# Performance work log

Measured on AMD Instinct MI355X. Metric: run time of the kernel, lower is better.

The kernel has to match this reference:

```python
import jax, jax.numpy as jnp
import numpy as np

N_NODES = 100000


def _gcn_conv(x, W, b, src, dst, n_nodes):
    """PyG GCNConv: linear -> symmetric norm (with self-loops) -> scatter-add -> bias."""
    h = x @ W  # [N, out]
    # add self-loops
    loop = jnp.arange(n_nodes, dtype=src.dtype)
    s = jnp.concatenate([src, loop])
    d = jnp.concatenate([dst, loop])
    # degree of target nodes (edge weight = 1)
    deg = jax.ops.segment_sum(jnp.ones_like(d, dtype=h.dtype), d, num_segments=n_nodes)
    dinv = jnp.where(deg > 0, jax.lax.rsqrt(jnp.maximum(deg, 1e-12)), 0.0)
    norm = dinv[s] * dinv[d]  # [E+N]
    msg = h[s] * norm[:, None]  # gather + scale
    out = jax.ops.segment_sum(msg, d, num_segments=n_nodes)
    return out + b


def setup_inputs() -> dict:
    key = jax.random.key(0)
    k1, k2, k3, k4 = jax.random.split(key, 4)
    F_IN, HID, OUT, E = 128, 16, 12, 3200000
    x = jax.random.normal(k1, (N_NODES, F_IN), dtype=jnp.float32)
    edge_index = jax.random.randint(k2, (2, E), 0, N_NODES, dtype=jnp.int64)
    W1 = jax.random.normal(k3, (F_IN, HID), dtype=jnp.float32) / np.sqrt(F_IN)
    b1 = jnp.zeros((HID,), dtype=jnp.float32)
    W2 = jax.random.normal(k4, (HID, OUT), dtype=jnp.float32) / np.sqrt(HID)
    b2 = jnp.zeros((OUT,), dtype=jnp.float32)
    return {"x": x, "edge_index": edge_index, "W1": W1, "b1": b1, "W2": W2, "b2": b2}


def reference(x, edge_index, W1, b1, W2, b2):
    src, dst = edge_index[0], edge_index[1]
    h = _gcn_conv(x, W1, b1, src, dst, N_NODES)
    h = jax.nn.relu(h)
    # dropout is identity at inference
    h = _gcn_conv(h, W2, b2, src, dst, N_NODES)
    return jax.nn.log_softmax(h, axis=1)
```

## Files before the change

### kernel.cpp

```cpp
#include <hip/hip_runtime.h>
#include <hip/hip_fp16.h>

#define N_FIN 128
#define N_HID 16
#define N_OUT 12
#define NBLK  1024
#define BN    512
#define STCAP 3200
#define SCAP  17152

__global__ __launch_bounds__(256) void k_binsort(const int* __restrict__ src,
                                                 const int* __restrict__ dst,
                                                 unsigned* __restrict__ hist,
                                                 unsigned* __restrict__ lstart,
                                                 unsigned* __restrict__ entries,
                                                 int E, int chunk, int NB) {
  __shared__ unsigned lh[256];
  __shared__ unsigned cur[256];
  __shared__ unsigned stage[STCAP];
  int t = threadIdx.x, blk = blockIdx.x;
  for (int b = t; b < NB; b += 256) lh[b] = 0u;
  __syncthreads();
  int clo = blk * chunk, chi = min(E, clo + chunk);
  for (int j = clo + t; j < chi; j += 256) atomicAdd(&lh[dst[j] >> 9], 1u);
  __syncthreads();
  unsigned v = (t < NB) ? lh[t] : 0u;
  cur[t] = v;
  __syncthreads();
#pragma unroll
  for (int off = 1; off < 256; off <<= 1) {
    unsigned y = (t >= off) ? cur[t - off] : 0u;
    __syncthreads();
    cur[t] += y;
    __syncthreads();
  }
  unsigned excl = cur[t] - v;
  if (t < NB) {
    hist[(size_t)t * NBLK + blk]   = v;
    lstart[(size_t)t * NBLK + blk] = excl;
  }
  cur[t] = excl;
  __syncthreads();
  for (int j = clo + t; j < chi; j += 256) {
    int d = dst[j];
    int b = d >> 9;
    unsigned p = atomicAdd(&cur[b], 1u);
    stage[p] = ((unsigned)src[j] << 9) | (unsigned)(d & (BN - 1));
  }
  __syncthreads();
  int n = chi - clo;
  for (int i = t; i < n; i += 256) entries[clo + i] = stage[i];
}

__global__ __launch_bounds__(256) void k_scan1(const unsigned* __restrict__ in,
                                               unsigned* __restrict__ out,
                                               unsigned* __restrict__ bsum, int M) {
  __shared__ unsigned s[256];
  int t = threadIdx.x, i = blockIdx.x * 256 + t;
  unsigned v = (i < M) ? in[i] : 0u;
  s[t] = v;
  __syncthreads();
#pragma unroll
  for (int off = 1; off < 256; off <<= 1) {
    unsigned y = (t >= off) ? s[t - off] : 0u;
    __syncthreads();
    s[t] += y;
    __syncthreads();
  }
  if (i < M) out[i] = s[t] - v;
  if (t == 255) bsum[blockIdx.x] = s[255];
}

__global__ __launch_bounds__(1024) void k_scan2(unsigned* __restrict__ bsum, int nb) {
  __shared__ unsigned s[1024];
  int t = threadIdx.x;
  unsigned v = (t < nb) ? bsum[t] : 0u;
  s[t] = v;
  __syncthreads();
#pragma unroll
  for (int off = 1; off < 1024; off <<= 1) {
    unsigned y = (t >= off) ? s[t - off] : 0u;
    __syncthreads();
    s[t] += y;
    __syncthreads();
  }
  if (t < nb) bsum[t] = s[t] - v;
}

__global__ __launch_bounds__(256) void k_scan3(unsigned* __restrict__ out,
                                               const unsigned* __restrict__ bsum, int M) {
  int i = blockIdx.x * 256 + threadIdx.x;
  if (i < M) out[i] += bsum[blockIdx.x];
}

__device__ __forceinline__ int frag_search(const unsigned* cum, unsigned i) {
  int lo = 0, hi = 1024;
  while (hi - lo > 1) { int mid = (lo + hi) >> 1; if (cum[mid] <= i) lo = mid; else hi = mid; }
  return lo;
}

__global__ __launch_bounds__(1024) void k_build(const unsigned* __restrict__ entries,
                                                const unsigned* __restrict__ base,
                                                const unsigned* __restrict__ lstart,
                                                unsigned* __restrict__ row_start,
                                                unsigned* __restrict__ deg,
                                                float* __restrict__ dinv,
                                                unsigned* __restrict__ esrc,
                                                int N, int NB, int E, int chunk) {
  __shared__ unsigned cum[1025];
  __shared__ unsigned lst[1024];
  __shared__ unsigned cnt[BN];
  __shared__ unsigned cur[BN];
  __shared__ unsigned raw[SCAP];
  __shared__ unsigned srt[SCAP];
  int t = threadIdx.x, b = blockIdx.x;
  unsigned bstart = base[(size_t)b * NBLK];
  unsigned bend = (b + 1 < NB) ? base[(size_t)(b + 1) * NBLK] : (unsigned)E;
  unsigned tot = bend - bstart;
  cum[t] = base[(size_t)b * NBLK + t] - bstart;
  lst[t] = lstart[(size_t)b * NBLK + t];
  if (t == 0) cum[1024] = tot;
  if (t < BN) cnt[t] = 0u;
  __syncthreads();
  bool fits = (tot <= SCAP);
  for (unsigned i = t; i < tot; i += 1024) {
    int f = frag_search(cum, i);
    unsigned en = entries[(size_t)f * chunk + lst[f] + (i - cum[f])];
    if (fits) raw[i] = en;
    atomicAdd(&cnt[en & (BN - 1)], 1u);
  }
  __syncthreads();
  unsigned v = (t < BN) ? cnt[t] : 0u;
  if (t < BN) cur[t] = v;
  __syncthreads();
#pragma unroll
  for (int off = 1; off < BN; off <<= 1) {
    unsigned y = (t < BN && t >= off) ? cur[t - off] : 0u;
    __syncthreads();
    if (t < BN) cur[t] += y;
    __syncthreads();
  }
  if (t < BN) {
    unsigned excl = cur[t] - v;
    cur[t] = fits ? excl : (bstart + excl);
    int node = b * BN + t;
    if (node < N) {
      row_start[node] = bstart + excl;
      deg[node] = v;
      dinv[node] = rsqrtf((float)(v + 1u));
    }
  }
  __syncthreads();
  if (fits) {
    for (unsigned i = t; i < tot; i += 1024) {
      unsigned en = raw[i];
      unsigned p = atomicAdd(&cur[en & (BN - 1)], 1u);
      srt[p] = en >> 9;
    }
    __syncthreads();
    for (unsigned i = t; i < tot; i += 1024) esrc[bstart + i] = srt[i];
  } else {
    for (unsigned i = t; i < tot; i += 1024) {
      int f = frag_search(cum, i);
      unsigned en = entries[(size_t)f * chunk + lst[f] + (i - cum[f])];
      unsigned p = atomicAdd(&cur[en & (BN - 1)], 1u);
      esrc[p] = en >> 9;
    }
  }
}

__global__ __launch_bounds__(256) void k_gemm1(const float* __restrict__ x,
                                               const float* __restrict__ W1,
                                               const float* __restrict__ dinv,
                                               __half* __restrict__ hs, int N) {
  __shared__ float xs[16][132];
  __shared__ float wT[16][132];
  int t = threadIdx.x;
#pragma unroll
  for (int i = 0; i < 8; ++i) {
    int idx = t + i * 256;
    int k = idx >> 4, c = idx & 15;
    wT[c][k] = W1[idx];
  }
  int row0 = blockIdx.x * 16;
#pragma unroll
  for (int i = 0; i < 2; ++i) {
    int idx = t + i * 256;
    int r = idx >> 5, c4 = idx & 31;
    float4 v = make_float4(0.f, 0.f, 0.f, 0.f);
    if (row0 + r < N) v = *(const float4*)(x + (size_t)(row0 + r) * N_FIN + c4 * 4);
    *(float4*)&xs[r][c4 * 4] = v;
  }
  __syncthreads();
  int col = t & 15, r = t >> 4;
  float acc = 0.f;
#pragma unroll
  for (int kc = 0; kc < 32; ++kc) {
    float4 xv = *(const float4*)&xs[r][kc * 4];
    float4 wv = *(const float4*)&wT[col][kc * 4];
    acc += xv.x * wv.x + xv.y * wv.y + xv.z * wv.z + xv.w * wv.w;
  }
  int row = row0 + r;
  if (row < N) hs[(size_t)row * N_HID + col] = __float2half(dinv[row] * acc);
}

__device__ __forceinline__ float4 h4f(uint2 v) {
  __half2 h0 = *(__half2*)&v.x, h1 = *(__half2*)&v.y;
  float2 f0 = __half22float2(h0), f1 = __half22float2(h1);
  return make_float4(f0.x, f0.y, f1.x, f1.y);
}
#define ACC(a, v) { float4 f = h4f(v); a.x += f.x; a.y += f.y; a.z += f.z; a.w += f.w; }

__global__ __launch_bounds__(256) void k_gagg1(const unsigned* __restrict__ esrc,
                                               const unsigned* __restrict__ row_start,
                                               const unsigned* __restrict__ deg,
                                               const uint2* __restrict__ hs,
                                               const float* __restrict__ dinv,
                                               const float* __restrict__ b1,
                                               const float* __restrict__ W2,
                                               __half* __restrict__ hs2, int N) {
  __shared__ float os[64][17];
  __shared__ float w2s[N_HID][N_OUT];
  __shared__ float b1s[N_HID];
  int t = threadIdx.x;
  if (t < N_HID * N_OUT) w2s[t / N_OUT][t % N_OUT] = W2[t];
  if (t < N_HID) b1s[t] = b1[t];
  __syncthreads();
  int nl = t >> 2, c4 = t & 3;
  int node = blockIdx.x * 64 + nl;
  if (node < N) {
    unsigned s0 = row_start[node], dn = deg[node];
    float4 a0 = make_float4(0.f, 0.f, 0.f, 0.f), a1 = a0, a2 = a0, a3 = a0;
    unsigned j = 0;
    for (; j + 8 <= dn; j += 8) {
      unsigned e0 = esrc[s0 + j],     e1 = esrc[s0 + j + 1];
      unsigned e2 = esrc[s0 + j + 2], e3 = esrc[s0 + j + 3];
      unsigned e4 = esrc[s0 + j + 4], e5 = esrc[s0 + j + 5];
      unsigned e6 = esrc[s0 + j + 6], e7 = esrc[s0 + j + 7];
      uint2 v0 = hs[(size_t)e0 * 4 + c4], v1 = hs[(size_t)e1 * 4 + c4];
      uint2 v2 = hs[(size_t)e2 * 4 + c4], v3 = hs[(size_t)e3 * 4 + c4];
      uint2 v4 = hs[(size_t)e4 * 4 + c4], v5 = hs[(size_t)e5 * 4 + c4];
      uint2 v6 = hs[(size_t)e6 * 4 + c4], v7 = hs[(size_t)e7 * 4 + c4];
      ACC(a0, v0); ACC(a1, v1); ACC(a2, v2); ACC(a3, v3);
      ACC(a0, v4); ACC(a1, v5); ACC(a2, v6); ACC(a3, v7);
    }
    for (; j < dn; ++j) {
      uint2 v = hs[(size_t)esrc[s0 + j] * 4 + c4];
      ACC(a0, v);
    }
    float4 sf = h4f(hs[(size_t)node * 4 + c4]);
    float di = dinv[node];
    int cb = c4 * 4;
    os[nl][cb + 0] = fmaxf(di * (a0.x + a1.x + a2.x + a3.x + sf.x) + b1s[cb + 0], 0.f);
    os[nl][cb + 1] = fmaxf(di * (a0.y + a1.y + a2.y + a3.y + sf.y) + b1s[cb + 1], 0.f);
    os[nl][cb + 2] = fmaxf(di * (a0.z + a1.z + a2.z + a3.z + sf.z) + b1s[cb + 2], 0.f);
    os[nl][cb + 3] = fmaxf(di * (a0.w + a1.w + a2.w + a3.w + sf.w) + b1s[cb + 3], 0.f);
  }
  __syncthreads();
  for (int idx = t; idx < 64 * 16; idx += 256) {
    int n2 = idx >> 4, cc = idx & 15;
    int node2 = blockIdx.x * 64 + n2;
    if (node2 < N) {
      float s = 0.f;
      if (cc < N_OUT) {
#pragma unroll
        for (int k = 0; k < N_HID; ++k) s += os[n2][k] * w2s[k][cc];
        s *= dinv[node2];
      }
      hs2[(size_t)node2 * N_HID + cc] = __float2half(s);
    }
  }
}

__global__ __launch_bounds__(256) void k_gagg2(const unsigned* __restrict__ esrc,
                                               const unsigned* __restrict__ row_start,
                                               const unsigned* __restrict__ deg,
                                               const uint2* __restrict__ hs2,
                                               const float* __restrict__ dinv,
                                               const float* __restrict__ b2,
                                               float* __restrict__ out, int N) {
  __shared__ float zs[64][13];
  __shared__ float ls[64];
  __shared__ float b2s[N_OUT];
  int t = threadIdx.x;
  if (t < N_OUT) b2s[t] = b2[t];
  __syncthreads();
  int nl = t >> 2, c4 = t & 3;
  int node = blockIdx.x * 64 + nl;
  if (node < N) {
    unsigned s0 = row_start[node], dn = deg[node];
    float4 a0 = make_float4(0.f, 0.f, 0.f, 0.f), a1 = a0, a2 = a0, a3 = a0;
    unsigned j = 0;
    for (; j + 8 <= dn; j += 8) {
      unsigned e0 = esrc[s0 + j],     e1 = esrc[s0 + j + 1];
      unsigned e2 = esrc[s0 + j + 2], e3 = esrc[s0 + j + 3];
      unsigned e4 = esrc[s0 + j + 4], e5 = esrc[s0 + j + 5];
      unsigned e6 = esrc[s0 + j + 6], e7 = esrc[s0 + j + 7];
      uint2 v0 = hs2[(size_t)e0 * 4 + c4], v1 = hs2[(size_t)e1 * 4 + c4];
      uint2 v2 = hs2[(size_t)e2 * 4 + c4], v3 = hs2[(size_t)e3 * 4 + c4];
      uint2 v4 = hs2[(size_t)e4 * 4 + c4], v5 = hs2[(size_t)e5 * 4 + c4];
      uint2 v6 = hs2[(size_t)e6 * 4 + c4], v7 = hs2[(size_t)e7 * 4 + c4];
      ACC(a0, v0); ACC(a1, v1); ACC(a2, v2); ACC(a3, v3);
      ACC(a0, v4); ACC(a1, v5); ACC(a2, v6); ACC(a3, v7);
    }
    for (; j < dn; ++j) {
      uint2 v = hs2[(size_t)esrc[s0 + j] * 4 + c4];
      ACC(a0, v);
    }
    if (c4 < 3) {
      float4 sf = h4f(hs2[(size_t)node * 4 + c4]);
      float di = dinv[node];
      int cb = c4 * 4;
      zs[nl][cb + 0] = di * (a0.x + a1.x + a2.x + a3.x + sf.x) + b2s[cb + 0];
      zs[nl][cb + 1] = di * (a0.y + a1.y + a2.y + a3.y + sf.y) + b2s[cb + 1];
      zs[nl][cb + 2] = di * (a0.z + a1.z + a2.z + a3.z + sf.z) + b2s[cb + 2];
      zs[nl][cb + 3] = di * (a0.w + a1.w + a2.w + a3.w + sf.w) + b2s[cb + 3];
    }
  }
  __syncthreads();
  if (t < 64) {
    int node2 = blockIdx.x * 64 + t;
    if (node2 < N) {
      float m = zs[t][0];
#pragma unroll
      for (int jj = 1; jj < N_OUT; ++jj) m = fmaxf(m, zs[t][jj]);
      float sum = 0.f;
#pragma unroll
      for (int jj = 0; jj < N_OUT; ++jj) sum += __expf(zs[t][jj] - m);
      ls[t] = m + __logf(sum);
    }
  }
  __syncthreads();
  for (int idx = t; idx < 64 * N_OUT; idx += 256) {
    int n2 = idx / N_OUT, cc = idx % N_OUT;
    int node2 = blockIdx.x * 64 + n2;
    if (node2 < N) out[(size_t)node2 * N_OUT + cc] = zs[n2][cc] - ls[n2];
  }
}

extern "C" void kernel_launch(void* const* d_in, const int* in_sizes, int n_in,
                              void* d_out, int out_size, void* d_ws, size_t ws_size,
                              hipStream_t stream) {
  const float* x  = (const float*)d_in[0];
  const int*   ei = (const int*)d_in[1];
  const float* W1 = (const float*)d_in[2];
  const float* b1 = (const float*)d_in[3];
  const float* W2 = (const float*)d_in[4];
  const float* b2 = (const float*)d_in[5];
  int N = in_sizes[0] / N_FIN;
  int E = in_sizes[1] / 2;
  const int* src = ei;
  const int* dst = ei + E;

  int NB = (N + BN - 1) / BN;
  int M  = NB * NBLK;
  int chunk = (E + NBLK - 1) / NBLK;
  int sb = (M + 255) / 256;

  char* ws = (char*)d_ws;
  unsigned* hist      = (unsigned*)ws;  ws += (size_t)M * 4;
  unsigned* base      = (unsigned*)ws;  ws += (size_t)M * 4;
  unsigned* lstart    = (unsigned*)ws;  ws += (size_t)M * 4;
  unsigned* bsum      = (unsigned*)ws;  ws += 4096;
  float*    dinv      = (float*)ws;     ws += (size_t)N * 4;
  unsigned* deg       = (unsigned*)ws;  ws += (size_t)N * 4;
  unsigned* row_start = (unsigned*)ws;  ws += (size_t)N * 4;
  size_t big_bytes = (size_t)E * 4;
  size_t hs_bytes  = (size_t)N * N_HID * 2 * 2;
  if (hs_bytes > big_bytes) big_bytes = hs_bytes;
  unsigned* entries = (unsigned*)ws;
  __half*   hs      = (__half*)ws;
  __half*   hs2     = (__half*)(ws + (size_t)N * N_HID * 2);
  ws += big_bytes;
  unsigned* esrc    = (unsigned*)ws;

  k_binsort<<<NBLK, 256, 0, stream>>>(src, dst, hist, lstart, entries, E, chunk, NB);
  k_scan1  <<<sb, 256, 0, stream>>>(hist, base, bsum, M);
  k_scan2  <<<1, 1024, 0, stream>>>(bsum, sb);
  k_scan3  <<<sb, 256, 0, stream>>>(base, bsum, M);
  k_build  <<<NB, 1024, 0, stream>>>(entries, base, lstart, row_start, deg, dinv, esrc,
                                     N, NB, E, chunk);
  k_gemm1  <<<(N + 15) / 16, 256, 0, stream>>>(x, W1, dinv, hs, N);
  k_gagg1  <<<(N + 63) / 64, 256, 0, stream>>>(esrc, row_start, deg, (const uint2*)hs,
                                               dinv, b1, W2, hs2, N);
  k_gagg2  <<<(N + 63) / 64, 256, 0, stream>>>(esrc, row_start, deg, (const uint2*)hs2,
                                               dinv, b2, (float*)d_out, N);
}
```

Baseline: 135.7 us.

## Drop global scan kernels, single-pass binsort, split aggregation across two sub-lanes

Binsort now reads src/dst once into shared staging, accumulates per-bucket totals with global atomics, and performs the local sort from shared memory. The three global prefix-scan kernels are removed; k_build recomputes the bucket prefix and the per-fragment prefix locally in shared memory. Row start and degree are packed into one uint2. Both aggregation kernels assign two sub-lanes per node with a stride-2 gather and reduce them through shared memory, using 32 nodes per block. This cuts launches and the global scan passes, and raises parallelism per node in the gather, at the cost of extra shared-memory reductions and redundant prefix work in every build block.

```diff
diff --git a/kernel.cpp b/kernel.cpp
--- a/kernel.cpp
+++ b/kernel.cpp
@@ -13,18 +13,27 @@
                                                  const int* __restrict__ dst,
                                                  unsigned* __restrict__ hist,
                                                  unsigned* __restrict__ lstart,
+                                                 unsigned* __restrict__ bucket_tot,
                                                  unsigned* __restrict__ entries,
                                                  int E, int chunk, int NB) {
   __shared__ unsigned lh[256];
   __shared__ unsigned cur[256];
   __shared__ unsigned stage[STCAP];
+  __shared__ unsigned srt[STCAP];
+  __shared__ unsigned char bid[STCAP];
   int t = threadIdx.x, blk = blockIdx.x;
-  for (int b = t; b < NB; b += 256) lh[b] = 0u;
-  __syncthreads();
-  int clo = blk * chunk, chi = min(E, clo + chunk);
-  for (int j = clo + t; j < chi; j += 256) atomicAdd(&lh[dst[j] >> 9], 1u);
-  __syncthreads();
-  unsigned v = (t < NB) ? lh[t] : 0u;
+  lh[t] = 0u;
+  __syncthreads();
+  int clo = blk * chunk, chi = min(E, clo + chunk), n = chi - clo;
+  for (int j = clo + t; j < chi; j += 256) {
+    int d = dst[j], s = src[j];
+    int b = d >> 9;
+    stage[j - clo] = ((unsigned)s << 9) | (unsigned)(d & (BN - 1));
+    bid[j - clo] = (unsigned char)b;
+    atomicAdd(&lh[b], 1u);
+  }
+  __syncthreads();
+  unsigned v = lh[t];
   cur[t] = v;
   __syncthreads();
 #pragma unroll
@@ -38,59 +47,16 @@
   if (t < NB) {
     hist[(size_t)t * NBLK + blk]   = v;
     lstart[(size_t)t * NBLK + blk] = excl;
+    if (v) atomicAdd(&bucket_tot[t], v);
   }
   cur[t] = excl;
   __syncthreads();
-  for (int j = clo + t; j < chi; j += 256) {
-    int d = dst[j];
-    int b = d >> 9;
-    unsigned p = atomicAdd(&cur[b], 1u);
-    stage[p] = ((unsigned)src[j] << 9) | (unsigned)(d & (BN - 1));
-  }
-  __syncthreads();
-  int n = chi - clo;
-  for (int i = t; i < n; i += 256) entries[clo + i] = stage[i];
-}
-
-__global__ __launch_bounds__(256) void k_scan1(const unsigned* __restrict__ in,
-                                               unsigned* __restrict__ out,
-                                               unsigned* __restrict__ bsum, int M) {
-  __shared__ unsigned s[256];
-  int t = threadIdx.x, i = blockIdx.x * 256 + t;
-  unsigned v = (i < M) ? in[i] : 0u;
-  s[t] = v;
-  __syncthreads();
-#pragma unroll
-  for (int off = 1; off < 256; off <<= 1) {
-    unsigned y = (t >= off) ? s[t - off] : 0u;
-    __syncthreads();
-    s[t] += y;
-    __syncthreads();
-  }
-  if (i < M) out[i] = s[t] - v;
-  if (t == 255) bsum[blockIdx.x] = s[255];
-}
-
-__global__ __launch_bounds__(1024) void k_scan2(unsigned* __restrict__ bsum, int nb) {
-  __shared__ unsigned s[1024];
-  int t = threadIdx.x;
-  unsigned v = (t < nb) ? bsum[t] : 0u;
-  s[t] = v;
-  __syncthreads();
-#pragma unroll
-  for (int off = 1; off < 1024; off <<= 1) {
-    unsigned y = (t >= off) ? s[t - off] : 0u;
-    __syncthreads();
-    s[t] += y;
-    __syncthreads();
-  }
-  if (t < nb) bsum[t] = s[t] - v;
-}
-
-__global__ __launch_bounds__(256) void k_scan3(unsigned* __restrict__ out,
-                                               const unsigned* __restrict__ bsum, int M) {
-  int i = blockIdx.x * 256 + threadIdx.x;
-  if (i < M) out[i] += bsum[blockIdx.x];
+  for (int i = t; i < n; i += 256) {
+    unsigned p = atomicAdd(&cur[bid[i]], 1u);
+    srt[p] = stage[i];
+  }
+  __syncthreads();
+  for (int i = t; i < n; i += 256) entries[clo + i] = srt[i];
 }
 
 __device__ __forceinline__ int frag_search(const unsigned* cum, unsigned i) {
@@ -100,10 +66,10 @@
 }
 
 __global__ __launch_bounds__(1024) void k_build(const unsigned* __restrict__ entries,
-                                                const unsigned* __restrict__ base,
+                                                const unsigned* __restrict__ hist,
                                                 const unsigned* __restrict__ lstart,
-                                                unsigned* __restrict__ row_start,
-                                                unsigned* __restrict__ deg,
+                                                const unsigned* __restrict__ bucket_tot,
+                                                uint2* __restrict__ rsd,
                                                 float* __restrict__ dinv,
                                                 unsigned* __restrict__ esrc,
                                                 int N, int NB, int E, int chunk) {
@@ -114,14 +80,36 @@
   __shared__ unsigned raw[SCAP];
   __shared__ unsigned srt[SCAP];
   int t = threadIdx.x, b = blockIdx.x;
-  unsigned bstart = base[(size_t)b * NBLK];
-  unsigned bend = (b + 1 < NB) ? base[(size_t)(b + 1) * NBLK] : (unsigned)E;
-  unsigned tot = bend - bstart;
-  cum[t] = base[(size_t)b * NBLK + t] - bstart;
+  if (t < 256) cur[t] = (t < NB) ? bucket_tot[t] : 0u;
+  __syncthreads();
+#pragma unroll
+  for (int off = 1; off < 256; off <<= 1) {
+    unsigned y = 0;
+    if (t < 256 && t >= off) y = cur[t - off];
+    __syncthreads();
+    if (t < 256) cur[t] += y;
+    __syncthreads();
+  }
+  unsigned bstart = (b == 0) ? 0u : cur[b - 1];
+  __syncthreads();
+  unsigned hv = hist[(size_t)b * NBLK + t];
   lst[t] = lstart[(size_t)b * NBLK + t];
-  if (t == 0) cum[1024] = tot;
+  cum[t] = hv;
+  __syncthreads();
+#pragma unroll
+  for (int off = 1; off < 1024; off <<= 1) {
+    unsigned y = (t >= off) ? cum[t - off] : 0u;
+    __syncthreads();
+    cum[t] += y;
+    __syncthreads();
+  }
+  unsigned incl = cum[t];
+  __syncthreads();
+  cum[t] = incl - hv;
+  if (t == 1023) cum[1024] = incl;
   if (t < BN) cnt[t] = 0u;
   __syncthreads();
+  unsigned tot = cum[1024];
   bool fits = (tot <= SCAP);
   for (unsigned i = t; i < tot; i += 1024) {
     int f = frag_search(cum, i);
@@ -145,8 +133,7 @@
     cur[t] = fits ? excl : (bstart + excl);
     int node = b * BN + t;
     if (node < N) {
-      row_start[node] = bstart + excl;
-      deg[node] = v;
+      rsd[node] = make_uint2(bstart + excl, v);
       dinv[node] = rsqrtf((float)(v + 1u));
     }
   }
@@ -212,59 +199,57 @@
 #define ACC(a, v) { float4 f = h4f(v); a.x += f.x; a.y += f.y; a.z += f.z; a.w += f.w; }
 
 __global__ __launch_bounds__(256) void k_gagg1(const unsigned* __restrict__ esrc,
-                                               const unsigned* __restrict__ row_start,
-                                               const unsigned* __restrict__ deg,
+                                               const uint2* __restrict__ rsd,
                                                const uint2* __restrict__ hs,
                                                const float* __restrict__ dinv,
                                                const float* __restrict__ b1,
                                                const float* __restrict__ W2,
                                                __half* __restrict__ hs2, int N) {
-  __shared__ float os[64][17];
+  __shared__ float os[32][2][16];
+  __shared__ float ro[32][17];
   __shared__ float w2s[N_HID][N_OUT];
   __shared__ float b1s[N_HID];
   int t = threadIdx.x;
   if (t < N_HID * N_OUT) w2s[t / N_OUT][t % N_OUT] = W2[t];
   if (t < N_HID) b1s[t] = b1[t];
-  __syncthreads();
-  int nl = t >> 2, c4 = t & 3;
-  int node = blockIdx.x * 64 + nl;
+  int nl = t >> 3, sub = (t >> 2) & 1, c4 = t & 3;
+  int node = blockIdx.x * 32 + nl;
   if (node < N) {
-    unsigned s0 = row_start[node], dn = deg[node];
+    uint2 rd = rsd[node];
+    unsigned s0 = rd.x, dn = rd.y;
     float4 a0 = make_float4(0.f, 0.f, 0.f, 0.f), a1 = a0, a2 = a0, a3 = a0;
-    unsigned j = 0;
-    for (; j + 8 <= dn; j += 8) {
-      unsigned e0 = esrc[s0 + j],     e1 = esrc[s0 + j + 1];
-      unsigned e2 = esrc[s0 + j + 2], e3 = esrc[s0 + j + 3];
-      unsigned e4 = esrc[s0 + j + 4], e5 = esrc[s0 + j + 5];
-      unsigned e6 = esrc[s0 + j + 6], e7 = esrc[s0 + j + 7];
+    unsigned j = (unsigned)sub;
+    for (; j + 6 < dn; j += 8) {
+      unsigned e0 = esrc[s0 + j],     e1 = esrc[s0 + j + 2];
+      unsigned e2 = esrc[s0 + j + 4], e3 = esrc[s0 + j + 6];
       uint2 v0 = hs[(size_t)e0 * 4 + c4], v1 = hs[(size_t)e1 * 4 + c4];
       uint2 v2 = hs[(size_t)e2 * 4 + c4], v3 = hs[(size_t)e3 * 4 + c4];
-      uint2 v4 = hs[(size_t)e4 * 4 + c4], v5 = hs[(size_t)e5 * 4 + c4];
-      uint2 v6 = hs[(size_t)e6 * 4 + c4], v7 = hs[(size_t)e7 * 4 + c4];
       ACC(a0, v0); ACC(a1, v1); ACC(a2, v2); ACC(a3, v3);
-      ACC(a0, v4); ACC(a1, v5); ACC(a2, v6); ACC(a3, v7);
-    }
-    for (; j < dn; ++j) {
-      uint2 v = hs[(size_t)esrc[s0 + j] * 4 + c4];
-      ACC(a0, v);
-    }
-    float4 sf = h4f(hs[(size_t)node * 4 + c4]);
-    float di = dinv[node];
+    }
+    for (; j < dn; j += 2) { uint2 v = hs[(size_t)esrc[s0 + j] * 4 + c4]; ACC(a0, v); }
+    if (sub == 0) { uint2 v = hs[(size_t)node * 4 + c4]; ACC(a0, v); }
     int cb = c4 * 4;
-    os[nl][cb + 0] = fmaxf(di * (a0.x + a1.x + a2.x + a3.x + sf.x) + b1s[cb + 0], 0.f);
-    os[nl][cb + 1] = fmaxf(di * (a0.y + a1.y + a2.y + a3.y + sf.y) + b1s[cb + 1], 0.f);
-    os[nl][cb + 2] = fmaxf(di * (a0.z + a1.z + a2.z + a3.z + sf.z) + b1s[cb + 2], 0.f);
-    os[nl][cb + 3] = fmaxf(di * (a0.w + a1.w + a2.w + a3.w + sf.w) + b1s[cb + 3], 0.f);
-  }
-  __syncthreads();
-  for (int idx = t; idx < 64 * 16; idx += 256) {
+    os[nl][sub][cb + 0] = a0.x + a1.x + a2.x + a3.x;
+    os[nl][sub][cb + 1] = a0.y + a1.y + a2.y + a3.y;
+    os[nl][sub][cb + 2] = a0.z + a1.z + a2.z + a3.z;
+    os[nl][sub][cb + 3] = a0.w + a1.w + a2.w + a3.w;
+  }
+  __syncthreads();
+  for (int idx = t; idx < 32 * 16; idx += 256) {
     int n2 = idx >> 4, cc = idx & 15;
-    int node2 = blockIdx.x * 64 + n2;
+    int node2 = blockIdx.x * 32 + n2;
+    if (node2 < N)
+      ro[n2][cc] = fmaxf(dinv[node2] * (os[n2][0][cc] + os[n2][1][cc]) + b1s[cc], 0.f);
+  }
+  __syncthreads();
+  for (int idx = t; idx < 32 * 16; idx += 256) {
+    int n2 = idx >> 4, cc = idx & 15;
+    int node2 = blockIdx.x * 32 + n2;
     if (node2 < N) {
       float s = 0.f;
       if (cc < N_OUT) {
 #pragma unroll
-        for (int k = 0; k < N_HID; ++k) s += os[n2][k] * w2s[k][cc];
+        for (int k = 0; k < N_HID; ++k) s += ro[n2][k] * w2s[k][cc];
         s *= dinv[node2];
       }
       hs2[(size_t)node2 * N_HID + cc] = __float2half(s);
@@ -273,53 +258,49 @@
 }
 
 __global__ __launch_bounds__(256) void k_gagg2(const unsigned* __restrict__ esrc,
-                                               const unsigned* __restrict__ row_start,
-                                               const unsigned* __restrict__ deg,
+                                               const uint2* __restrict__ rsd,
                                                const uint2* __restrict__ hs2,
                                                const float* __restrict__ dinv,
                                                const float* __restrict__ b2,
                                                float* __restrict__ out, int N) {
-  __shared__ float zs[64][13];
-  __shared__ float ls[64];
+  __shared__ float os[32][2][16];
+  __shared__ float zs[32][13];
+  __shared__ float ls[32];
   __shared__ float b2s[N_OUT];
   int t = threadIdx.x;
   if (t < N_OUT) b2s[t] = b2[t];
-  __syncthreads();
-  int nl = t >> 2, c4 = t & 3;
-  int node = blockIdx.x * 64 + nl;
+  int nl = t >> 3, sub = (t >> 2) & 1, c4 = t & 3;
+  int node = blockIdx.x * 32 + nl;
   if (node < N) {
-    unsigned s0 = row_start[node], dn = deg[node];
+    uint2 rd = rsd[node];
+    unsigned s0 = rd.x, dn = rd.y;
     float4 a0 = make_float4(0.f, 0.f, 0.f, 0.f), a1 = a0, a2 = a0, a3 = a0;
-    unsigned j = 0;
-    for (; j + 8 <= dn; j += 8) {
-      unsigned e0 = esrc[s0 + j],     e1 = esrc[s0 + j + 1];
-      unsigned e2 = esrc[s0 + j + 2], e3 = esrc[s0 + j + 3];
-      unsigned e4 = esrc[s0 + j + 4], e5 = esrc[s0 + j + 5];
-      unsigned e6 = esrc[s0 + j + 6], e7 = esrc[s0 + j + 7];
+    unsigned j = (unsigned)sub;
+    for (; j + 6 < dn; j += 8) {
+      unsigned e0 = esrc[s0 + j],     e1 = esrc[s0 + j + 2];
+      unsigned e2 = esrc[s0 + j + 4], e3 = esrc[s0 + j + 6];
       uint2 v0 = hs2[(size_t)e0 * 4 + c4], v1 = hs2[(size_t)e1 * 4 + c4];
       uint2 v2 = hs2[(size_t)e2 * 4 + c4], v3 = hs2[(size_t)e3 * 4 + c4];
-      uint2 v4 = hs2[(size_t)e4 * 4 + c4], v5 = hs2[(size_t)e5 * 4 + c4];
-      uint2 v6 = hs2[(size_t)e6 * 4 + c4], v7 = hs2[(size_t)e7 * 4 + c4];
       ACC(a0, v0); ACC(a1, v1); ACC(a2, v2); ACC(a3, v3);
-      ACC(a0, v4); ACC(a1, v5); ACC(a2, v6); ACC(a3, v7);
-    }
-    for (; j < dn; ++j) {
-      uint2 v = hs2[(size_t)esrc[s0 + j] * 4 + c4];
-      ACC(a0, v);
-    }
-    if (c4 < 3) {
-      float4 sf = h4f(hs2[(size_t)node * 4 + c4]);
-      float di = dinv[node];
-      int cb = c4 * 4;
-      zs[nl][cb + 0] = di * (a0.x + a1.x + a2.x + a3.x + sf.x) + b2s[cb + 0];
-      zs[nl][cb + 1] = di * (a0.y + a1.y + a2.y + a3.y + sf.y) + b2s[cb + 1];
-      zs[nl][cb + 2] = di * (a0.z + a1.z + a2.z + a3.z + sf.z) + b2s[cb + 2];
-      zs[nl][cb + 3] = di * (a0.w + a1.w + a2.w + a3.w + sf.w) + b2s[cb + 3];
-    }
-  }
-  __syncthreads();
-  if (t < 64) {
-    int node2 = blockIdx.x * 64 + t;
+    }
+    for (; j < dn; j += 2) { uint2 v = hs2[(size_t)esrc[s0 + j] * 4 + c4]; ACC(a0, v); }
+    if (sub == 0) { uint2 v = hs2[(size_t)node * 4 + c4]; ACC(a0, v); }
+    int cb = c4 * 4;
+    os[nl][sub][cb + 0] = a0.x + a1.x + a2.x + a3.x;
+    os[nl][sub][cb + 1] = a0.y + a1.y + a2.y + a3.y;
+    os[nl][sub][cb + 2] = a0.z + a1.z + a2.z + a3.z;
+    os[nl][sub][cb + 3] = a0.w + a1.w + a2.w + a3.w;
+  }
+  __syncthreads();
+  for (int idx = t; idx < 32 * N_OUT; idx += 256) {
+    int n2 = idx / N_OUT, cc = idx % N_OUT;
+    int node2 = blockIdx.x * 32 + n2;
+    if (node2 < N)
+      zs[n2][cc] = dinv[node2] * (os[n2][0][cc] + os[n2][1][cc]) + b2s[cc];
+  }
+  __syncthreads();
+  if (t < 32) {
+    int node2 = blockIdx.x * 32 + t;
     if (node2 < N) {
       float m = zs[t][0];
 #pragma unroll
@@ -331,9 +312,9 @@
     }
   }
   __syncthreads();
-  for (int idx = t; idx < 64 * N_OUT; idx += 256) {
+  for (int idx = t; idx < 32 * N_OUT; idx += 256) {
     int n2 = idx / N_OUT, cc = idx % N_OUT;
-    int node2 = blockIdx.x * 64 + n2;
+    int node2 = blockIdx.x * 32 + n2;
     if (node2 < N) out[(size_t)node2 * N_OUT + cc] = zs[n2][cc] - ls[n2];
   }
 }
@@ -355,16 +336,13 @@
   int NB = (N + BN - 1) / BN;
   int M  = NB * NBLK;
   int chunk = (E + NBLK - 1) / NBLK;
-  int sb = (M + 255) / 256;
 
   char* ws = (char*)d_ws;
-  unsigned* hist      = (unsigned*)ws;  ws += (size_t)M * 4;
-  unsigned* base      = (unsigned*)ws;  ws += (size_t)M * 4;
-  unsigned* lstart    = (unsigned*)ws;  ws += (size_t)M * 4;
-  unsigned* bsum      = (unsigned*)ws;  ws += 4096;
-  float*    dinv      = (float*)ws;     ws += (size_t)N * 4;
-  unsigned* deg       = (unsigned*)ws;  ws += (size_t)N * 4;
-  unsigned* row_start = (unsigned*)ws;  ws += (size_t)N * 4;
+  unsigned* hist       = (unsigned*)ws;  ws += (size_t)M * 4;
+  unsigned* lstart     = (unsigned*)ws;  ws += (size_t)M * 4;
+  unsigned* bucket_tot = (unsigned*)ws;  ws += 1024;
+  float*    dinv       = (float*)ws;     ws += (size_t)N * 4;
+  uint2*    rsd        = (uint2*)ws;     ws += (size_t)N * 8;
   size_t big_bytes = (size_t)E * 4;
   size_t hs_bytes  = (size_t)N * N_HID * 2 * 2;
   if (hs_bytes > big_bytes) big_bytes = hs_bytes;
@@ -374,15 +352,13 @@
   ws += big_bytes;
   unsigned* esrc    = (unsigned*)ws;
 
-  k_binsort<<<NBLK, 256, 0, stream>>>(src, dst, hist, lstart, entries, E, chunk, NB);
-  k_scan1  <<<sb, 256, 0, stream>>>(hist, base, bsum, M);
-  k_scan2  <<<1, 1024, 0, stream>>>(bsum, sb);
-  k_scan3  <<<sb, 256, 0, stream>>>(base, bsum, M);
-  k_build  <<<NB, 1024, 0, stream>>>(entries, base, lstart, row_start, deg, dinv, esrc,
+  hipMemsetAsync(bucket_tot, 0, 1024, stream);
+  k_binsort<<<NBLK, 256, 0, stream>>>(src, dst, hist, lstart, bucket_tot, entries, E, chunk, NB);
+  k_build  <<<NB, 1024, 0, stream>>>(entries, hist, lstart, bucket_tot, rsd, dinv, esrc,
                                      N, NB, E, chunk);
   k_gemm1  <<<(N + 15) / 16, 256, 0, stream>>>(x, W1, dinv, hs, N);
-  k_gagg1  <<<(N + 63) / 64, 256, 0, stream>>>(esrc, row_start, deg, (const uint2*)hs,
+  k_gagg1  <<<(N + 31) / 32, 256, 0, stream>>>(esrc, rsd, (const uint2*)hs,
                                                dinv, b1, W2, hs2, N);
-  k_gagg2  <<<(N + 63) / 64, 256, 0, stream>>>(esrc, row_start, deg, (const uint2*)hs2,
+  k_gagg2  <<<(N + 31) / 32, 256, 0, stream>>>(esrc, rsd, (const uint2*)hs2,
                                                dinv, b2, (float*)d_out, N);
 }
```

Result: no change. 137.6 us (+1.4%).
